# Kernel optimization log

Hardware: AMD Instinct MI355X
Metric: run time of the kernel (lower is better)

Reference implementation:

```python
import jax, jax.numpy as jnp
import numpy as np

P_PTS = 131072
N_TRI = 256


def _dot(a, b):
    return (a * b).sum(-1)


def _dot2(a):
    return (a * a).sum(-1)


def setup_inputs() -> dict:
    key = jax.random.key(0)
    k1, k2 = jax.random.split(key)
    p = jax.random.normal(k1, (P_PTS, 3), dtype=jnp.float32)
    # matches 0.3 * rand(n,3,3) - 0.15 initialization of the parameter
    points = 0.3 * jax.random.uniform(k2, (N_TRI, 3, 3), dtype=jnp.float32) - 0.15
    return {"p": p, "points": points}


def reference(p, points):
    # points: [n,3,3] -> vertices A,B,C of each triangle
    A, B, C = points[:, 0], points[:, 1], points[:, 2]  # [n,3]
    # edges (points - roll(points,1,dims=-2)) rows: A-C, B-A, C-B
    ac, ba, cb = A - C, B - A, C - B                     # [n,3]
    nor = jnp.cross(ba, ac)                              # [n,3]

    pa = p[:, None, :] - A[None]                         # [P,n,3]
    pb = p[:, None, :] - B[None]
    pc = p[:, None, :] - C[None]

    sidedness = (jnp.sign(_dot(jnp.cross(ba, nor)[None], pa))
                 + jnp.sign(_dot(jnp.cross(cb, nor)[None], pb))
                 + jnp.sign(_dot(jnp.cross(ac, nor)[None], pc)))  # [P,n]

    def seg_dist2(e, pv):
        # squared distance from pv to segment along edge e
        t = jnp.clip(_dot(e[None], pv) / _dot2(e)[None], 0.0, 1.0)  # [P,n]
        d = e[None] * t[..., None] - pv                              # [P,n,3]
        return _dot2(d)                                              # [P,n]

    same_sided = jnp.minimum(jnp.minimum(seg_dist2(ba, pa), seg_dist2(cb, pb)),
                             seg_dist2(ac, pc))                      # [P,n]
    opp_sided = jnp.square(_dot(nor[None], pa)) / _dot2(nor)[None]   # [P,n]

    d = jnp.sqrt(jnp.maximum(jnp.where(sidedness < 2.0, same_sided, opp_sided), 1e-8))
    d = d - 0.04                                                     # [P,n]

    k = 32.0  # smooth-min sharpness
    out = -jnp.log(jnp.maximum(jnp.exp(-k * d).sum(-1), 1e-6)) / k   # [P]
    return out[:, None]
```

## Files before the change

kernel.cpp:

```cpp
#include <hip/hip_runtime.h>

#define N_PTS   131072
#define FAR_CONST 0.4317347049363836f
#define CUT2 0.8227f


__global__ __launch_bounds__(1024) void classify_kernel(
    const float* __restrict__ p, const float* __restrict__ points,
    float* __restrict__ out, int* __restrict__ counter, int* __restrict__ cidx,
    float* __restrict__ cpx, float* __restrict__ cpy, float* __restrict__ cpz,
    float* __restrict__ tri)
{
    const int tid = threadIdx.x;

    if (blockIdx.x == 0 && tid < 256) {
        const int t = tid;
        const float* tp = points + t * 9;
        float Ax = tp[0], Ay = tp[1], Az = tp[2];
        float Bx = tp[3], By = tp[4], Bz = tp[5];
        float Cx = tp[6], Cy = tp[7], Cz = tp[8];

        float acx = Ax - Cx, acy = Ay - Cy, acz = Az - Cz;
        float bax = Bx - Ax, bay = By - Ay, baz = Bz - Az;
        float cbx = Cx - Bx, cby = Cy - By, cbz = Cz - Bz;

        float nx = bay * acz - baz * acy;
        float ny = baz * acx - bax * acz;
        float nz = bax * acy - bay * acx;
        float nsq = nx * nx + ny * ny + nz * nz;
        float inn = 1.0f / nsq;
        float rn  = sqrtf(inn);

        float c1x = bay * nz - baz * ny, c1y = baz * nx - bax * nz, c1z = bax * ny - bay * nx;
        float c2x = cby * nz - cbz * ny, c2y = cbz * nx - cbx * nz, c2z = cbx * ny - cby * nx;

        tri[ 0*256+t] = bax; tri[ 1*256+t] = bay; tri[ 2*256+t] = baz;
        tri[ 3*256+t] = -(bax * Ax + bay * Ay + baz * Az);
        tri[ 4*256+t] = cbx; tri[ 5*256+t] = cby; tri[ 6*256+t] = cbz;
        tri[ 7*256+t] = -(cbx * Bx + cby * By + cbz * Bz);
        tri[ 8*256+t] = acx; tri[ 9*256+t] = acy; tri[10*256+t] = acz;
        tri[11*256+t] = -(acx * Cx + acy * Cy + acz * Cz);
        tri[12*256+t] = c1x * inn; tri[13*256+t] = c1y * inn; tri[14*256+t] = c1z * inn;
        tri[15*256+t] = -(c1x * Ax + c1y * Ay + c1z * Az) * inn;
        tri[16*256+t] = c2x * inn; tri[17*256+t] = c2y * inn; tri[18*256+t] = c2z * inn;
        tri[19*256+t] = -(c2x * Bx + c2y * By + c2z * Bz) * inn;
        tri[20*256+t] = nx * rn; tri[21*256+t] = ny * rn; tri[22*256+t] = nz * rn;
        tri[23*256+t] = -(nx * Ax + ny * Ay + nz * Az) * rn;
        tri[24*256+t] = -2.0f * Ax; tri[25*256+t] = -2.0f * Ay; tri[26*256+t] = -2.0f * Az;
        tri[27*256+t] = Ax * Ax + Ay * Ay + Az * Az;
        float basq = bax * bax + bay * bay + baz * baz;
        float cbsq = cbx * cbx + cby * cby + cbz * cbz;
        float acsq = acx * acx + acy * acy + acz * acz;
        tri[28*256+t] = basq; tri[29*256+t] = cbsq; tri[30*256+t] = acsq;
        tri[31*256+t] = 1.0f / basq; tri[32*256+t] = 1.0f / cbsq; tri[33*256+t] = 1.0f / acsq;
    }

    const int i = blockIdx.x * 1024 + tid;
    const float px = p[3 * i + 0];
    const float py = p[3 * i + 1];
    const float pz = p[3 * i + 2];
    const float psq = fmaf(px, px, fmaf(py, py, pz * pz));

    out[i] = FAR_CONST;

    const bool near = psq < CUT2;
    const unsigned long long mask = __ballot(near);
    const int lane = tid & 63;
    const int wv   = tid >> 6;

    __shared__ int wcnt[16];
    __shared__ int woff[16];
    __shared__ int sbase;
    if (lane == 0) wcnt[wv] = __popcll(mask);
    __syncthreads();
    if (tid == 0) {
        int tot = 0;
#pragma unroll
        for (int w = 0; w < 16; ++w) { woff[w] = tot; tot += wcnt[w]; }
        sbase = atomicAdd(counter, tot);
    }
    __syncthreads();

    if (near) {
        const int rank = __popcll(mask & ((1ull << lane) - 1));
        const int slot = sbase + woff[wv] + rank;
        cidx[slot] = i;
        cpx[slot] = px; cpy[slot] = py; cpz[slot] = pz;
    }
}

template <int CTRL>
static __device__ __forceinline__ float row_ror_f(float x) {
    int r = __builtin_amdgcn_update_dpp(
        0, __builtin_bit_cast(int, x), CTRL, 0xF, 0xF, true);
    return __builtin_bit_cast(float, r);
}

__global__ __launch_bounds__(256, 4) void tri_main_kernel(
    const float* __restrict__ tri, const int* __restrict__ counter,
    const int* __restrict__ cidx,
    const float* __restrict__ cpx, const float* __restrict__ cpy,
    const float* __restrict__ cpz, float* __restrict__ out)
{
    const int count = *counter;
    const int gbase = blockIdx.x * 32;
    if (gbase >= count) return;

    __shared__ float red[4][2][64];

    const int tid  = threadIdx.x;
    const int lane = tid & 63;
    const int wv   = tid >> 6;
    const int l15  = lane & 15;
    const int t    = wv * 64 + lane;

    const float ba_x = tri[ 0*256+t], ba_y = tri[ 1*256+t], ba_z = tri[ 2*256+t];
    const float K1   = tri[ 3*256+t];
    const float cb_x = tri[ 4*256+t], cb_y = tri[ 5*256+t], cb_z = tri[ 6*256+t];
    const float K2   = tri[ 7*256+t];
    const float ac_x = tri[ 8*256+t], ac_y = tri[ 9*256+t], ac_z = tri[10*256+t];
    const float K3   = tri[11*256+t];
    const float c1_x = tri[12*256+t], c1_y = tri[13*256+t], c1_z = tri[14*256+t];
    const float Ks1  = tri[15*256+t];
    const float c2_x = tri[16*256+t], c2_y = tri[17*256+t], c2_z = tri[18*256+t];
    const float Ks2  = tri[19*256+t];
    const float un_x = tri[20*256+t], un_y = tri[21*256+t], un_z = tri[22*256+t];
    const float Kun  = tri[23*256+t];
    const float mA_x = tri[24*256+t], mA_y = tri[25*256+t], mA_z = tri[26*256+t];
    const float KA   = tri[27*256+t];
    const float basq = tri[28*256+t], cbsq = tri[29*256+t], acsq = tri[30*256+t];
    const float ib   = tri[31*256+t], ic = tri[32*256+t], ia = tri[33*256+t];

    const float EK = -46.166241308446834f;
    const float EB = 1.8466496523378732f;

    float accA = 0.0f;
    float accB = 0.0f;

#define TRI_BODY(J, ACC)                                                      \
    {                                                                         \
        const int jj = (J);                                                   \
        const float px = cpx[gbase + jj];                                     \
        const float py = cpy[gbase + jj];                                     \
        const float pz = cpz[gbase + jj];                                     \
        const float psq = fmaf(px, px, fmaf(py, py, pz * pz));                \
                                                                              \
        float q1 = fmaf(ba_x, px, fmaf(ba_y, py, fmaf(ba_z, pz, K1)));        \
        float q2 = fmaf(cb_x, px, fmaf(cb_y, py, fmaf(cb_z, pz, K2)));        \
        float q3 = fmaf(ac_x, px, fmaf(ac_y, py, fmaf(ac_z, pz, K3)));        \
        float s1 = fmaf(c1_x, px, fmaf(c1_y, py, fmaf(c1_z, pz, Ks1)));       \
        float s2 = fmaf(c2_x, px, fmaf(c2_y, py, fmaf(c2_z, pz, Ks2)));       \
        float dn = fmaf(un_x, px, fmaf(un_y, py, fmaf(un_z, pz, Kun)));       \
                                                                              \
        float pasq = psq + fmaf(mA_x, px, fmaf(mA_y, py, fmaf(mA_z, pz, KA)));\
        float pbsq = fmaf(-2.0f, q1, pasq) + basq;                            \
        float pcsq = fmaf(-2.0f, q2, pbsq) + cbsq;                            \
                                                                              \
        float s3 = (1.0f - s1) - s2;                                          \
                                                                              \
        float t1 = __builtin_amdgcn_fmed3f(q1 * ib, 0.0f, 1.0f);              \
        float w1 = fmaf(-t1, basq, q1);                                       \
        float e1 = fmaf(-t1, q1 + w1, pasq);                                  \
                                                                              \
        float t2 = __builtin_amdgcn_fmed3f(q2 * ic, 0.0f, 1.0f);              \
        float w2 = fmaf(-t2, cbsq, q2);                                       \
        float e2 = fmaf(-t2, q2 + w2, pbsq);                                  \
                                                                              \
        float t3 = __builtin_amdgcn_fmed3f(q3 * ia, 0.0f, 1.0f);              \
        float w3 = fmaf(-t3, acsq, q3);                                       \
        float e3 = fmaf(-t3, q3 + w3, pcsq);                                  \
                                                                              \
        float same = fminf(fminf(e1, e2), e3);                                \
        float opp  = dn * dn;                                                 \
                                                                              \
        float mn  = fminf(fminf(s1, s2), s3);                                 \
        float med = __builtin_amdgcn_fmed3f(s1, s2, s3);                      \
        bool inside = (med > 0.0f) & (mn >= 0.0f);                            \
        float qv = inside ? opp : same;                                       \
                                                                              \
        float dd = __builtin_amdgcn_sqrtf(fmaxf(qv, 1e-8f));                  \
        float term = __builtin_amdgcn_exp2f(fmaf(dd, EK, EB));                \
                                                                              \
         \
                                                     \
        term += row_ror_f<0x121>(term);                                       \
        term += row_ror_f<0x122>(term);                                       \
        term += row_ror_f<0x124>(term);                                       \
        term += row_ror_f<0x128>(term);                                       \
                           \
        ACC = (l15 == (jj & 15)) ? ACC + term : ACC;                          \
    }

#pragma unroll 4
    for (int j0 = 0; j0 < 16; ++j0)  TRI_BODY(j0, accA)
#pragma unroll 4
    for (int j1 = 16; j1 < 32; ++j1) TRI_BODY(j1, accB)
#undef TRI_BODY

    red[wv][0][lane] = accA;
    red[wv][1][lane] = accB;
    __syncthreads();

    if (tid < 32) {
        const int s = gbase + tid;
        if (s < count) {
            const int sel = tid >> 4;
            const int col = tid & 15;
            float total = 0.0f;
#pragma unroll
            for (int w = 0; w < 4; ++w) {
                float rw = ((red[w][sel][ 0 + col] + red[w][sel][16 + col]) +
                            (red[w][sel][32 + col] + red[w][sel][48 + col]));
                total += rw;
            }
            out[cidx[s]] =
                -__builtin_amdgcn_logf(fmaxf(total, 1e-6f)) * 0.02166084939249829f;
        }
    }
}

extern "C" void kernel_launch(void* const* d_in, const int* in_sizes, int n_in,
                              void* d_out, int out_size, void* d_ws, size_t ws_size,
                              hipStream_t stream) {
    const float* p      = (const float*)d_in[0];
    const float* points = (const float*)d_in[1];
    float* out          = (float*)d_out;

    int*   counter = (int*)d_ws;
    int*   cidx    = counter + 2;
    float* cpx     = (float*)(cidx + N_PTS);
    float* cpy     = cpx + N_PTS;
    float* cpz     = cpy + N_PTS;
    float* tri     = cpz + N_PTS;

    (void)hipMemsetAsync(counter, 0, sizeof(int), stream);

    hipLaunchKernelGGL(classify_kernel, dim3(N_PTS / 1024), dim3(1024), 0, stream,
                       p, points, out, counter, cidx, cpx, cpy, cpz, tri);

    hipLaunchKernelGGL(tri_main_kernel, dim3(N_PTS / 32), dim3(256), 0, stream,
                       tri, counter, cidx, cpx, cpy, cpz, out);
}
```

Baseline: 70.57 us.

## Use persistent grid-stride blocks and pack compacted points as float4

The main triangle kernel now launches a fixed grid of 1024 blocks that loop over 32-point groups with a grid stride, instead of one block per possible group, most of which exited early. Each block loads its 34 per-triangle constants once and reuses them across groups, which avoids launching thousands of empty blocks. Compacted near points are stored as one float4 per point instead of three separate float arrays, so each point is fetched with a single vector load. An extra __syncthreads per iteration guards reuse of the shared reduction buffer.

Measured after the change: 72.95 us. 1.03x slower.

```diff
diff --git a/kernel.cpp b/kernel.cpp
--- a/kernel.cpp
+++ b/kernel.cpp
@@ -8,8 +8,7 @@
 __global__ __launch_bounds__(1024) void classify_kernel(
     const float* __restrict__ p, const float* __restrict__ points,
     float* __restrict__ out, int* __restrict__ counter, int* __restrict__ cidx,
-    float* __restrict__ cpx, float* __restrict__ cpy, float* __restrict__ cpz,
-    float* __restrict__ tri)
+    float4* __restrict__ cpt, float* __restrict__ tri)
 {
     const int tid = threadIdx.x;
 
@@ -85,7 +84,7 @@
         const int rank = __popcll(mask & ((1ull << lane) - 1));
         const int slot = sbase + woff[wv] + rank;
         cidx[slot] = i;
-        cpx[slot] = px; cpy[slot] = py; cpz[slot] = pz;
+        cpt[slot] = make_float4(px, py, pz, 0.0f);
     }
 }
 
@@ -98,14 +97,10 @@
 
 __global__ __launch_bounds__(256, 4) void tri_main_kernel(
     const float* __restrict__ tri, const int* __restrict__ counter,
-    const int* __restrict__ cidx,
-    const float* __restrict__ cpx, const float* __restrict__ cpy,
-    const float* __restrict__ cpz, float* __restrict__ out)
+    const int* __restrict__ cidx, const float4* __restrict__ cpt,
+    float* __restrict__ out)
 {
     const int count = *counter;
-    const int gbase = blockIdx.x * 32;
-    if (gbase >= count) return;
-
     __shared__ float red[4][2][64];
 
     const int tid  = threadIdx.x;
@@ -134,15 +129,16 @@
     const float EK = -46.166241308446834f;
     const float EB = 1.8466496523378732f;
 
-    float accA = 0.0f;
-    float accB = 0.0f;
+    for (int gbase = blockIdx.x * 32; gbase < count; gbase += gridDim.x * 32) {
+
+        float accA = 0.0f;
+        float accB = 0.0f;
 
 #define TRI_BODY(J, ACC)                                                      \
     {                                                                         \
         const int jj = (J);                                                   \
-        const float px = cpx[gbase + jj];                                     \
-        const float py = cpy[gbase + jj];                                     \
-        const float pz = cpz[gbase + jj];                                     \
+        const float4 pt = cpt[gbase + jj];        \
+        const float px = pt.x, py = pt.y, pz = pt.z;                          \
         const float psq = fmaf(px, px, fmaf(py, py, pz * pz));                \
                                                                               \
         float q1 = fmaf(ba_x, px, fmaf(ba_y, py, fmaf(ba_z, pz, K1)));        \
@@ -192,30 +188,32 @@
     }
 
 #pragma unroll 4
-    for (int j0 = 0; j0 < 16; ++j0)  TRI_BODY(j0, accA)
+        for (int j0 = 0; j0 < 16; ++j0)  TRI_BODY(j0, accA)
 #pragma unroll 4
-    for (int j1 = 16; j1 < 32; ++j1) TRI_BODY(j1, accB)
+        for (int j1 = 16; j1 < 32; ++j1) TRI_BODY(j1, accB)
 #undef TRI_BODY
 
-    red[wv][0][lane] = accA;
-    red[wv][1][lane] = accB;
-    __syncthreads();
-
-    if (tid < 32) {
-        const int s = gbase + tid;
-        if (s < count) {
-            const int sel = tid >> 4;
-            const int col = tid & 15;
-            float total = 0.0f;
+        red[wv][0][lane] = accA;
+        red[wv][1][lane] = accB;
+        __syncthreads();
+
+        if (tid < 32) {
+            const int s = gbase + tid;
+            if (s < count) {
+                const int sel = tid >> 4;
+                const int col = tid & 15;
+                float total = 0.0f;
 #pragma unroll
-            for (int w = 0; w < 4; ++w) {
-                float rw = ((red[w][sel][ 0 + col] + red[w][sel][16 + col]) +
-                            (red[w][sel][32 + col] + red[w][sel][48 + col]));
-                total += rw;
+                for (int w = 0; w < 4; ++w) {
+                    float rw = ((red[w][sel][ 0 + col] + red[w][sel][16 + col]) +
+                                (red[w][sel][32 + col] + red[w][sel][48 + col]));
+                    total += rw;
+                }
+                out[cidx[s]] =
+                    -__builtin_amdgcn_logf(fmaxf(total, 1e-6f)) * 0.02166084939249829f;
             }
-            out[cidx[s]] =
-                -__builtin_amdgcn_logf(fmaxf(total, 1e-6f)) * 0.02166084939249829f;
         }
+        __syncthreads();
     }
 }
 
@@ -226,18 +224,16 @@
     const float* points = (const float*)d_in[1];
     float* out          = (float*)d_out;
 
-    int*   counter = (int*)d_ws;
-    int*   cidx    = counter + 2;
-    float* cpx     = (float*)(cidx + N_PTS);
-    float* cpy     = cpx + N_PTS;
-    float* cpz     = cpy + N_PTS;
-    float* tri     = cpz + N_PTS;
+    int*    counter = (int*)d_ws;
+    int*    cidx    = counter + 2;
+    float4* cpt     = (float4*)(cidx + N_PTS + 2);
+    float*  tri     = (float*)(cpt + N_PTS);
 
     (void)hipMemsetAsync(counter, 0, sizeof(int), stream);
 
     hipLaunchKernelGGL(classify_kernel, dim3(N_PTS / 1024), dim3(1024), 0, stream,
-                       p, points, out, counter, cidx, cpx, cpy, cpz, tri);
-
-    hipLaunchKernelGGL(tri_main_kernel, dim3(N_PTS / 32), dim3(256), 0, stream,
-                       tri, counter, cidx, cpx, cpy, cpz, out);
-}
+                       p, points, out, counter, cidx, cpt, tri);
+
+    hipLaunchKernelGGL(tri_main_kernel, dim3(1024), dim3(256), 0, stream,
+                       tri, counter, cidx, cpt, out);
+}
```
